# Performance work log

Measured on AMD Instinct MI355X. Metric: run time of the kernel, lower is better.

Reference implementation:

```python
import jax, jax.numpy as jnp
import numpy as np

B, L, D, H = 2, 2048, 1024, 16
P = D // H  # head dim = 64


def setup_inputs() -> dict:
    key = jax.random.key(0)
    ks = jax.random.split(key, 9)
    s = 1.0 / np.sqrt(D)
    x = jax.random.normal(ks[0], (B, L, D), dtype=jnp.float32)
    Wq = jax.random.normal(ks[1], (D, D), dtype=jnp.float32) * s
    bq = jax.random.normal(ks[2], (D,), dtype=jnp.float32) * 0.02
    Wk = jax.random.normal(ks[3], (D, D), dtype=jnp.float32) * s
    bk = jax.random.normal(ks[4], (D,), dtype=jnp.float32) * 0.02
    Wv = jax.random.normal(ks[5], (D, D), dtype=jnp.float32) * s
    bv = jax.random.normal(ks[6], (D,), dtype=jnp.float32) * 0.02
    Wo = jax.random.normal(ks[7], (D, D), dtype=jnp.float32) * s
    bo = jax.random.normal(ks[8], (D,), dtype=jnp.float32) * 0.02
    return {"token_activations": x, "Wq": Wq, "bq": bq, "Wk": Wk, "bk": bk,
            "Wv": Wv, "bv": bv, "Wo": Wo, "bo": bo}


def _split_heads(t):
    # 'b l (h p) -> b h l p'
    b, l, d = t.shape
    return t.reshape(b, l, H, P).transpose(0, 2, 1, 3)


def reference(token_activations, Wq, bq, Wk, bk, Wv, bv, Wo, bo):
    x = token_activations
    q = _split_heads(x @ Wq.T + bq)  # [B,H,L,P]
    k = _split_heads(x @ Wk.T + bk)
    v = _split_heads(x @ Wv.T + bv)
    # pattern[b,h,l,m] = K_l . Q_m / sqrt(P)
    scores = jnp.einsum('bhlp,bhmp->bhlm', k, q) / jnp.sqrt(jnp.float32(P))
    attn = jax.nn.softmax(scores, axis=-2)  # softmax over key axis l
    # out at query position m: sum_l attn[l,m] * V_l
    o = jnp.einsum('bhlm,bhlp->bhmp', attn, v)  # [B,H,L,P] (m indexed)
    o = o.transpose(0, 2, 1, 3).reshape(x.shape[0], x.shape[1], D)  # 'b h m p -> b m (h p)'
    return o @ Wo.T + bo
```

## Files before the change

### kernel.cpp

```cpp
#include <hip/hip_runtime.h>

typedef unsigned short u16;
typedef float f32x4 __attribute__((ext_vector_type(4)));
typedef __bf16 bf16x8 __attribute__((ext_vector_type(8)));
typedef __bf16 bf16x4 __attribute__((ext_vector_type(4)));

#define DEV static __device__ __forceinline__

constexpr int kB = 2;
constexpr int kL = 2048;
constexpr int kD = 1024;
constexpr int kH = 16;
constexpr int kP = 64;
constexpr int kM = kB * kL;
constexpr float kQScale = 0.125f * 1.44269504088896f;

DEV u16 f2bf(float x) {
  union { float f; unsigned u; } v;
  v.f = x;
  unsigned r = v.u + 0x7fffu + ((v.u >> 16) & 1u);
  return (u16)(r >> 16);
}

DEV void gload16(const void* g, void* l) {
  __builtin_amdgcn_global_load_lds(
      (const __attribute__((address_space(1))) unsigned int*)g,
      (__attribute__((address_space(3))) unsigned int*)l, 16, 0, 0);
}

__global__ void cvt_all(const float* __restrict__ x,
                        const float* __restrict__ w0, const float* __restrict__ w1,
                        const float* __restrict__ w2, const float* __restrict__ w3,
                        u16* __restrict__ xb,
                        u16* __restrict__ o0, u16* __restrict__ o1,
                        u16* __restrict__ o2, u16* __restrict__ o3) {
  int i = blockIdx.x * blockDim.x + threadIdx.x;
  const float* src;
  u16* dst;
  int j;
  if (i < (1 << 20)) {
    src = x; dst = xb; j = i;
  } else {
    int s = (i >> 18) & 3;
    j = i & ((1 << 18) - 1);
    src = s == 0 ? w0 : (s == 1 ? w1 : (s == 2 ? w2 : w3));
    dst = s == 0 ? o0 : (s == 1 ? o1 : (s == 2 ? o2 : o3));
  }
  float4 v = reinterpret_cast<const float4*>(src)[j];
  uint2 o;
  o.x = (unsigned)f2bf(v.x) | ((unsigned)f2bf(v.y) << 16);
  o.y = (unsigned)f2bf(v.z) | ((unsigned)f2bf(v.w) << 16);
  reinterpret_cast<uint2*>(dst)[j] = o;
}

template <bool SWAP>
DEV void gemm_tile(const u16* __restrict__ A, const u16* __restrict__ W,
                   int m0, int n0, u16* As, u16* Bs, f32x4 acc[4][4]) {
  const int tid = threadIdx.x;
  const int w = tid >> 6, lane = tid & 63;
  const int wr = w >> 1, wc = w & 1;
  const int g = lane >> 4, c = lane & 15;
  const int srow = lane >> 2;
  const int skoff = ((lane & 3) ^ (srow & 3)) * 8;
  const int rsl0 = (g ^ (c & 3)) * 8;

  for (int k0 = 0; k0 < kD; k0 += 32) {
    __syncthreads();
#pragma unroll
    for (int j = 0; j < 2; ++j) {
      const u16* ga = A + (size_t)(m0 + w * 32 + j * 16 + srow) * kD + k0 + skoff;
      gload16(ga, As + (w * 32 + j * 16) * 32);
      const u16* gb = W + (size_t)(n0 + w * 32 + j * 16 + srow) * kD + k0 + skoff;
      gload16(gb, Bs + (w * 32 + j * 16) * 32);
    }
    __syncthreads();

    bf16x8 af[4], bfr[4];
#pragma unroll
    for (int f = 0; f < 4; ++f) {
      af[f]  = *reinterpret_cast<const bf16x8*>(As + (wr * 64 + f * 16 + c) * 32 + rsl0);
      bfr[f] = *reinterpret_cast<const bf16x8*>(Bs + (wc * 64 + f * 16 + c) * 32 + rsl0);
    }
#pragma unroll
    for (int fi = 0; fi < 4; ++fi)
#pragma unroll
      for (int fj = 0; fj < 4; ++fj) {
        if constexpr (SWAP)
          acc[fj][fi] = __builtin_amdgcn_mfma_f32_16x16x32_bf16(bfr[fj], af[fi], acc[fj][fi], 0, 0, 0);
        else
          acc[fi][fj] = __builtin_amdgcn_mfma_f32_16x16x32_bf16(af[fi], bfr[fj], acc[fi][fj], 0, 0, 0);
      }
  }
}

__global__ __launch_bounds__(256) void qkv_kernel(
    const u16* __restrict__ xb,
    const u16* __restrict__ wq, const u16* __restrict__ wk, const u16* __restrict__ wv,
    const float* __restrict__ bq, const float* __restrict__ bk, const float* __restrict__ bv,
    u16* __restrict__ qb, u16* __restrict__ kb, u16* __restrict__ vtb) {
  __shared__ u16 As[128 * 32], Bs[128 * 32];
  const int hw = blockIdx.x;
  const int logical = (hw & 7) * 96 + (hw >> 3);
  const int mb = logical & 31, nb = logical >> 5;
  const int sel = nb >> 3;
  const int m0 = mb * 128, n0 = (nb & 7) * 128;
  const u16* W = sel == 0 ? wq : (sel == 1 ? wk : wv);
  const float* bias = sel == 0 ? bq : (sel == 1 ? bk : bv);

  const int lane = threadIdx.x & 63, w = threadIdx.x >> 6;
  const int wr = w >> 1, wc = w & 1, g = lane >> 4, c = lane & 15;
  const int bb = m0 >> 11;
  const int lbase = (m0 & 2047) + wr * 64;

  f32x4 acc[4][4];
#pragma unroll
  for (int i = 0; i < 4; ++i)
#pragma unroll
    for (int j = 0; j < 4; ++j) acc[i][j] = f32x4{0.f, 0.f, 0.f, 0.f};

  if (sel < 2) {
    gemm_tile<true>(xb, W, m0, n0, As, Bs, acc);
    u16* dst = sel == 0 ? qb : kb;
    const float scale = (sel == 0) ? kQScale : 1.0f;
#pragma unroll
    for (int fj = 0; fj < 4; ++fj) {
      const int n4 = n0 + wc * 64 + fj * 16 + g * 4;
      const float4 b4 = *reinterpret_cast<const float4*>(&bias[n4]);
      const int hh = n4 >> 6, p0 = n4 & 63;
      u16* base = dst + ((size_t)(bb * kH + hh)) * kL * kP + p0;
#pragma unroll
      for (int fi = 0; fi < 4; ++fi) {
        const int l = lbase + fi * 16 + c;
        bf16x4 o;
        o[0] = (__bf16)((acc[fj][fi][0] + b4.x) * scale);
        o[1] = (__bf16)((acc[fj][fi][1] + b4.y) * scale);
        o[2] = (__bf16)((acc[fj][fi][2] + b4.z) * scale);
        o[3] = (__bf16)((acc[fj][fi][3] + b4.w) * scale);
        *reinterpret_cast<bf16x4*>(base + (size_t)l * kP) = o;
      }
    }
  } else {
    gemm_tile<false>(xb, W, m0, n0, As, Bs, acc);
#pragma unroll
    for (int fj = 0; fj < 4; ++fj) {
      const int n = n0 + wc * 64 + fj * 16 + c;
      const float bv_ = bias[n];
      const int hh = n >> 6, p = n & 63;
      u16* base = vtb + (((size_t)(bb * kH + hh)) * kP + p) * kL;
#pragma unroll
      for (int fi = 0; fi < 4; ++fi) {
        const int l4 = lbase + fi * 16 + g * 4;
        bf16x4 o;
#pragma unroll
        for (int r = 0; r < 4; ++r) o[r] = (__bf16)(acc[fi][fj][r] + bv_);
        *reinterpret_cast<bf16x4*>(base + l4) = o;
      }
    }
  }
}

__global__ __launch_bounds__(512) void out_kernel(
    const u16* __restrict__ ob, const u16* __restrict__ wo,
    const float* __restrict__ bo, float* __restrict__ out) {
  __shared__ u16 As[128 * 32], Bs[128 * 32];
  const int hw = blockIdx.x;
  const int logical = (hw & 7) * 32 + (hw >> 3);
  const int m0 = (logical & 31) * 128, n0 = (logical >> 5) * 128;

  const int tid = threadIdx.x;
  const int w = tid >> 6, lane = tid & 63;
  const int wr = w >> 2, wc = w & 3;
  const int g = lane >> 4, c = lane & 15;
  const int srow = lane >> 2;
  const int skoff = ((lane & 3) ^ (srow & 3)) * 8;
  const int rsl0 = (g ^ (c & 3)) * 8;

  f32x4 acc[2][4];
#pragma unroll
  for (int i = 0; i < 2; ++i)
#pragma unroll
    for (int j = 0; j < 4; ++j) acc[i][j] = f32x4{0.f, 0.f, 0.f, 0.f};

  for (int k0 = 0; k0 < kD; k0 += 32) {
    __syncthreads();
    {
      const u16* ga = ob + (size_t)(m0 + w * 16 + srow) * kD + k0 + skoff;
      gload16(ga, As + (w * 16) * 32);
      const u16* gb = wo + (size_t)(n0 + w * 16 + srow) * kD + k0 + skoff;
      gload16(gb, Bs + (w * 16) * 32);
    }
    __syncthreads();

    bf16x8 af[4], bfr[2];
#pragma unroll
    for (int f = 0; f < 4; ++f)
      af[f] = *reinterpret_cast<const bf16x8*>(As + (wr * 64 + f * 16 + c) * 32 + rsl0);
#pragma unroll
    for (int f = 0; f < 2; ++f)
      bfr[f] = *reinterpret_cast<const bf16x8*>(Bs + (wc * 32 + f * 16 + c) * 32 + rsl0);
#pragma unroll
    for (int fj = 0; fj < 2; ++fj)
#pragma unroll
      for (int fi = 0; fi < 4; ++fi)
        acc[fj][fi] = __builtin_amdgcn_mfma_f32_16x16x32_bf16(bfr[fj], af[fi], acc[fj][fi], 0, 0, 0);
  }

#pragma unroll
  for (int fj = 0; fj < 2; ++fj) {
    const int n4 = n0 + wc * 32 + fj * 16 + g * 4;
    const float4 b4 = *reinterpret_cast<const float4*>(&bo[n4]);
#pragma unroll
    for (int fi = 0; fi < 4; ++fi) {
      const int m = m0 + wr * 64 + fi * 16 + c;
      float4 o;
      o.x = acc[fj][fi][0] + b4.x;
      o.y = acc[fj][fi][1] + b4.y;
      o.z = acc[fj][fi][2] + b4.z;
      o.w = acc[fj][fi][3] + b4.w;
      *reinterpret_cast<float4*>(&out[(size_t)m * kD + n4]) = o;
    }
  }
}

__global__ __launch_bounds__(512, 2) void attn_kernel(
    const u16* __restrict__ qb, const u16* __restrict__ kb,
    const u16* __restrict__ vtb, u16* __restrict__ ob) {
  __shared__ __align__(16) char kvs[2][2][8192];
  __shared__ __align__(16) char pts[8][2048];
  const int tid = threadIdx.x, w = tid >> 6, lane = tid & 63;
  const int g = lane >> 4, c = lane & 15;
  const int h = blockIdx.y, b = blockIdx.z;
  const size_t hoff = ((size_t)(b * kH + h)) * kL * kP;
  const char* Qg = (const char*)(qb + hoff);
  const char* Kg = (const char*)(kb + hoff);
  const char* Vg = (const char*)(vtb + hoff);
  const int q0 = blockIdx.x * 128 + w * 16;

  const int lrow = lane >> 3;
  const int spb = ((lane & 7) ^ lrow) << 4;
  const char* kp = Kg + (size_t)(w * 8 + lrow) * 128 + spb;
  const char* vp = Vg + (size_t)(w * 8 + lrow) * (kL * 2) + spb;

  auto stage = [&](int buf) {
    gload16(kp, &kvs[buf][0][w * 1024]);
    gload16(vp, &kvs[buf][1][w * 1024]);
    kp += 64 * 128;
    vp += 128;
  };

  const int csw = (c & 7) << 4;
  const int kvb0 = c * 128 + ((g * 16) ^ csw);
  const int kvb1 = c * 128 + ((64 + g * 16) ^ csw);
  char* myPt = &pts[w][0];

  bf16x8 qf[2];
#pragma unroll
  for (int kc = 0; kc < 2; ++kc)
    qf[kc] = *reinterpret_cast<const bf16x8*>(Qg + (size_t)(q0 + c) * 128 + kc * 64 + g * 16);

  f32x4 oacc[4];
#pragma unroll
  for (int pt = 0; pt < 4; ++pt) oacc[pt] = f32x4{0.f, 0.f, 0.f, 0.f};
  float Srun = 0.f;

  stage(0);
  __syncthreads();

  constexpr int NT = kL / 64;
  auto body = [&](int cur, int t) {
    if (t + 1 < NT) stage(cur ^ 1);
    const char* Ks = &kvs[cur][0][0];
    const char* Vs = &kvs[cur][1][0];

    f32x4 s[4];
    __builtin_amdgcn_s_setprio(1);
#pragma unroll
    for (int lt = 0; lt < 4; ++lt) {
      bf16x8 k0 = *reinterpret_cast<const bf16x8*>(Ks + lt * 2048 + kvb0);
      bf16x8 k1 = *reinterpret_cast<const bf16x8*>(Ks + lt * 2048 + kvb1);
      f32x4 z = f32x4{0.f, 0.f, 0.f, 0.f};
      z = __builtin_amdgcn_mfma_f32_16x16x32_bf16(k0, qf[0], z, 0, 0, 0);
      z = __builtin_amdgcn_mfma_f32_16x16x32_bf16(k1, qf[1], z, 0, 0, 0);
      s[lt] = z;
    }
    __builtin_amdgcn_s_setprio(0);

    float tsum = 0.f;
#pragma unroll
    for (int lt = 0; lt < 4; ++lt) {
      bf16x4 pv;
#pragma unroll
      for (int r = 0; r < 4; ++r) {
        float p = __builtin_amdgcn_exp2f(s[lt][r]);
        tsum += p;
        pv[r] = (__bf16)p;
      }
      *reinterpret_cast<bf16x4*>(myPt + c * 128 + ((lt * 32 + g * 8) ^ csw)) = pv;
    }
    Srun += tsum;

    bf16x8 pf0 = *reinterpret_cast<const bf16x8*>(myPt + kvb0);
    bf16x8 pf1 = *reinterpret_cast<const bf16x8*>(myPt + kvb1);
    __builtin_amdgcn_s_setprio(1);
#pragma unroll
    for (int pt = 0; pt < 4; ++pt) {
      bf16x8 v0 = *reinterpret_cast<const bf16x8*>(Vs + pt * 2048 + kvb0);
      bf16x8 v1 = *reinterpret_cast<const bf16x8*>(Vs + pt * 2048 + kvb1);
      oacc[pt] = __builtin_amdgcn_mfma_f32_16x16x32_bf16(pf0, v0, oacc[pt], 0, 0, 0);
      oacc[pt] = __builtin_amdgcn_mfma_f32_16x16x32_bf16(pf1, v1, oacc[pt], 0, 0, 0);
    }
    __builtin_amdgcn_s_setprio(0);
    __syncthreads();
  };

  for (int t = 0; t < NT; t += 2) {
    body(0, t);
    body(1, t + 1);
  }

  Srun += __shfl_xor(Srun, 16, 64);
  Srun += __shfl_xor(Srun, 32, 64);

  float rs = 1.f / Srun;
  float fr[4];
#pragma unroll
  for (int r = 0; r < 4; ++r) fr[r] = __shfl(rs, g * 4 + r, 64);
#pragma unroll
  for (int pt = 0; pt < 4; ++pt)
#pragma unroll
    for (int r = 0; r < 4; ++r) {
      int q = q0 + g * 4 + r;
      ob[((size_t)(b * kL + q)) * kD + h * kP + pt * 16 + c] = f2bf(oacc[pt][r] * fr[r]);
    }
}

extern "C" void kernel_launch(void* const* d_in, const int* in_sizes, int n_in,
                              void* d_out, int out_size, void* d_ws, size_t ws_size,
                              hipStream_t stream) {
  (void)in_sizes; (void)n_in; (void)out_size; (void)ws_size;
  const float* x  = (const float*)d_in[0];
  const float* Wq = (const float*)d_in[1];
  const float* bq = (const float*)d_in[2];
  const float* Wk = (const float*)d_in[3];
  const float* bk = (const float*)d_in[4];
  const float* Wv = (const float*)d_in[5];
  const float* bv = (const float*)d_in[6];
  const float* Wo = (const float*)d_in[7];
  const float* bo = (const float*)d_in[8];
  float* out = (float*)d_out;

  char* ws = (char*)d_ws;
  u16* xb  = (u16*)(ws);
  u16* wqb = (u16*)(ws + (8u << 20));
  u16* wkb = (u16*)(ws + (10u << 20));
  u16* wvb = (u16*)(ws + (12u << 20));
  u16* wob = (u16*)(ws + (14u << 20));
  u16* qb  = (u16*)(ws + (16u << 20));
  u16* kb  = (u16*)(ws + (24u << 20));
  u16* vtb = (u16*)(ws + (32u << 20));

  cvt_all<<<8192, 256, 0, stream>>>(x, Wq, Wk, Wv, Wo, xb, wqb, wkb, wvb, wob);

  qkv_kernel<<<768, 256, 0, stream>>>(
      xb, wqb, wkb, wvb, bq, bk, bv, qb, kb, vtb);

  attn_kernel<<<dim3(kL / 128, kH, kB), 512, 0, stream>>>(qb, kb, vtb, xb);

  out_kernel<<<256, 512, 0, stream>>>(xb, wob, bo, out);
}
```

Before: 116.2 us.

## Split attention key range in two with separate combine kernel

Attention work is split across the key dimension into two halves, which doubles the grid. Each half writes its unnormalized bf16 output and its per-query exp-sum to workspace. A new combine kernel adds the two partials and normalizes them before the output projection, and the workspace layout is rearranged so the second partial buffer reuses the weight-conversion region. The aim is more parallelism in the attention stage. In exchange it adds an extra launch, extra global traffic and bf16 rounding of the partial sums.

Measured after the change: 123.2 us. 6.0% more time.

```diff
diff --git a/kernel.cpp b/kernel.cpp
--- a/kernel.cpp
+++ b/kernel.cpp
@@ -20,6 +20,12 @@
   v.f = x;
   unsigned r = v.u + 0x7fffu + ((v.u >> 16) & 1u);
   return (u16)(r >> 16);
+}
+
+DEV float bf2f(u16 x) {
+  union { unsigned u; float f; } v;
+  v.u = (unsigned)x << 16;
+  return v.f;
 }
 
 DEV void gload16(const void* g, void* l) {
@@ -224,22 +230,26 @@
 
 __global__ __launch_bounds__(512, 2) void attn_kernel(
     const u16* __restrict__ qb, const u16* __restrict__ kb,
-    const u16* __restrict__ vtb, u16* __restrict__ ob) {
+    const u16* __restrict__ vtb, u16* __restrict__ ob0, u16* __restrict__ ob1,
+    float* __restrict__ Sp) {
   __shared__ __align__(16) char kvs[2][2][8192];
   __shared__ __align__(16) char pts[8][2048];
   const int tid = threadIdx.x, w = tid >> 6, lane = tid & 63;
   const int g = lane >> 4, c = lane & 15;
-  const int h = blockIdx.y, b = blockIdx.z;
+  const int h = blockIdx.y;
+  const int b = blockIdx.z >> 1, s = blockIdx.z & 1;
   const size_t hoff = ((size_t)(b * kH + h)) * kL * kP;
   const char* Qg = (const char*)(qb + hoff);
   const char* Kg = (const char*)(kb + hoff);
   const char* Vg = (const char*)(vtb + hoff);
   const int q0 = blockIdx.x * 128 + w * 16;
+  const int l00 = s * 1024;
+  u16* obp = s == 0 ? ob0 : ob1;
 
   const int lrow = lane >> 3;
   const int spb = ((lane & 7) ^ lrow) << 4;
-  const char* kp = Kg + (size_t)(w * 8 + lrow) * 128 + spb;
-  const char* vp = Vg + (size_t)(w * 8 + lrow) * (kL * 2) + spb;
+  const char* kp = Kg + (size_t)(l00 + w * 8 + lrow) * 128 + spb;
+  const char* vp = Vg + (size_t)(w * 8 + lrow) * (kL * 2) + (size_t)l00 * 2 + spb;
 
   auto stage = [&](int buf) {
     gload16(kp, &kvs[buf][0][w * 1024]);
@@ -266,13 +276,13 @@
   stage(0);
   __syncthreads();
 
-  constexpr int NT = kL / 64;
+  constexpr int NT = 1024 / 64;
   auto body = [&](int cur, int t) {
     if (t + 1 < NT) stage(cur ^ 1);
     const char* Ks = &kvs[cur][0][0];
     const char* Vs = &kvs[cur][1][0];
 
-    f32x4 s[4];
+    f32x4 sc[4];
     __builtin_amdgcn_s_setprio(1);
 #pragma unroll
     for (int lt = 0; lt < 4; ++lt) {
@@ -281,7 +291,7 @@
       f32x4 z = f32x4{0.f, 0.f, 0.f, 0.f};
       z = __builtin_amdgcn_mfma_f32_16x16x32_bf16(k0, qf[0], z, 0, 0, 0);
       z = __builtin_amdgcn_mfma_f32_16x16x32_bf16(k1, qf[1], z, 0, 0, 0);
-      s[lt] = z;
+      sc[lt] = z;
     }
     __builtin_amdgcn_s_setprio(0);
 
@@ -291,7 +301,7 @@
       bf16x4 pv;
 #pragma unroll
       for (int r = 0; r < 4; ++r) {
-        float p = __builtin_amdgcn_exp2f(s[lt][r]);
+        float p = __builtin_amdgcn_exp2f(sc[lt][r]);
         tsum += p;
         pv[r] = (__bf16)p;
       }
@@ -320,18 +330,38 @@
 
   Srun += __shfl_xor(Srun, 16, 64);
   Srun += __shfl_xor(Srun, 32, 64);
-
-  float rs = 1.f / Srun;
-  float fr[4];
-#pragma unroll
-  for (int r = 0; r < 4; ++r) fr[r] = __shfl(rs, g * 4 + r, 64);
+  if (lane < 16)
+    Sp[(((size_t)(s * kB + b)) * kH + h) * kL + q0 + c] = Srun;
+
 #pragma unroll
   for (int pt = 0; pt < 4; ++pt)
 #pragma unroll
     for (int r = 0; r < 4; ++r) {
       int q = q0 + g * 4 + r;
-      ob[((size_t)(b * kL + q)) * kD + h * kP + pt * 16 + c] = f2bf(oacc[pt][r] * fr[r]);
-    }
+      obp[((size_t)(b * kL + q)) * kD + h * kP + pt * 16 + c] = f2bf(oacc[pt][r]);
+    }
+}
+
+__global__ void combine_kernel(u16* __restrict__ o0, const u16* __restrict__ o1,
+                               const float* __restrict__ Sp) {
+  int i = blockIdx.x * blockDim.x + threadIdx.x;
+  size_t base = (size_t)i * 8;
+  int col = (int)(base & 1023);
+  int h = col >> 6;
+  int row = (int)(base >> 10);
+  int b = row >> 11, l = row & 2047;
+  float S0 = Sp[(((size_t)b) * kH + h) * kL + l];
+  float S1 = Sp[(((size_t)(kB + b)) * kH + h) * kL + l];
+  float rs = 1.f / (S0 + S1);
+  uint4 a  = *reinterpret_cast<const uint4*>(o0 + base);
+  uint4 b4 = *reinterpret_cast<const uint4*>(o1 + base);
+  const u16* ap = (const u16*)&a;
+  const u16* bp = (const u16*)&b4;
+  uint4 o;
+  u16* op = (u16*)&o;
+#pragma unroll
+  for (int j = 0; j < 8; ++j) op[j] = f2bf((bf2f(ap[j]) + bf2f(bp[j])) * rs);
+  *reinterpret_cast<uint4*>(o0 + base) = o;
 }
 
 extern "C" void kernel_launch(void* const* d_in, const int* in_sizes, int n_in,
@@ -351,20 +381,25 @@
 
   char* ws = (char*)d_ws;
   u16* xb  = (u16*)(ws);
-  u16* wqb = (u16*)(ws + (8u << 20));
-  u16* wkb = (u16*)(ws + (10u << 20));
-  u16* wvb = (u16*)(ws + (12u << 20));
-  u16* wob = (u16*)(ws + (14u << 20));
-  u16* qb  = (u16*)(ws + (16u << 20));
-  u16* kb  = (u16*)(ws + (24u << 20));
-  u16* vtb = (u16*)(ws + (32u << 20));
+  u16* wob = (u16*)(ws + (8u << 20));
+  u16* ob1 = (u16*)(ws + (10u << 20));
+  u16* wqb = (u16*)(ws + (10u << 20));
+  u16* wkb = (u16*)(ws + (12u << 20));
+  u16* wvb = (u16*)(ws + (14u << 20));
+  u16* qb  = (u16*)(ws + (18u << 20));
+  u16* kb  = (u16*)(ws + (26u << 20));
+  u16* vtb = (u16*)(ws + (34u << 20));
+  float* Sp = (float*)(ws + (42u << 20));
 
   cvt_all<<<8192, 256, 0, stream>>>(x, Wq, Wk, Wv, Wo, xb, wqb, wkb, wvb, wob);
 
   qkv_kernel<<<768, 256, 0, stream>>>(
       xb, wqb, wkb, wvb, bq, bk, bv, qb, kb, vtb);
 
-  attn_kernel<<<dim3(kL / 128, kH, kB), 512, 0, stream>>>(qb, kb, vtb, xb);
+  attn_kernel<<<dim3(kL / 128, kH, kB * 2), 512, 0, stream>>>(
+      qb, kb, vtb, xb, ob1, Sp);
+
+  combine_kernel<<<2048, 256, 0, stream>>>(xb, ob1, Sp);
 
   out_kernel<<<256, 512, 0, stream>>>(xb, wob, bo, out);
 }
```
